# Kernel optimization log

Measured on AMD Instinct MI355X. Metric: run time of the kernel, lower is better.

The kernel has to match this reference:

```python
import jax
jax.config.update("jax_enable_x64", True)
import jax.numpy as jnp
import numpy as np

# --- Field setup -------------------------------------------------------------
# The original uses BLS12-381 Fr (255-bit Montgomery limbs). JAX has no native
# 256-bit ints, so the reference uses an NTT-friendly 31-bit prime with the
# same algorithmic structure (two-adic radix-2 INTT, grand products, MSM-style
# commitment reduction). Products of two residues fit in int64.
P = 2013265921          # 15 * 2^27 + 1, two-adicity 27
G = 31                  # generator of F_P^*
LOG_N = 20
N = 1 << LOG_N
W = pow(G, (P - 1) // N, P)      # primitive N-th root of unity
W_INV = pow(W, P - 2, P)
N_INV = pow(N, P - 2, P)
K1, K2, K3 = 7, 13, 17           # PLONK coset shifts for wire identities


def _bitrev_perm(n):
    logn = n.bit_length() - 1
    idx = np.arange(n, dtype=np.int64)
    rev = np.zeros(n, dtype=np.int64)
    for i in range(logn):
        rev = (rev << 1) | ((idx >> i) & 1)
    return rev


def _twiddles(n, root):
    logn = n.bit_length() - 1
    out = []
    for s in range(1, logn + 1):
        m = 1 << s
        wm = pow(root, n // m, P)
        half = m >> 1
        ws = np.empty(half, dtype=np.int64)
        w = 1
        for k in range(half):
            ws[k] = w
            w = (w * wm) % P
        out.append(jnp.asarray(ws))
    return out

_BREV = jnp.asarray(_bitrev_perm(N))
_TW_INV = _twiddles(N, W_INV)


def _ntt_core(a, tw):
    # iterative radix-2 Cooley-Tukey, fully vectorized per stage
    n = a.shape[0]
    a = a[_BREV]
    for s, ws in enumerate(tw):
        half = 1 << s
        a = a.reshape(-1, 2 * half)         # [n/(2*half), 2*half]
        u = a[:, :half]
        t = (a[:, half:] * ws[None, :]) % P
        a = jnp.concatenate([(u + t) % P, (u - t) % P], axis=1)
    return a.reshape(n)


def intt(evals):
    # inverse NTT: evaluations on the domain -> coefficients (nn.Intt)
    return (_ntt_core(evals, _TW_INV) * N_INV) % P


def inv_mod(x):
    # batch modular inverse: x^(P-2), exponent is a compile-time constant
    e = P - 2
    res = jnp.ones_like(x)
    base = x % P
    while e:
        if e & 1:
            res = (res * base) % P
        base = (base * base) % P
        e >>= 1
    return res


def cumprod_mod(x):
    return jax.lax.associative_scan(lambda a, b: (a * b) % P, x)


def shifted_cumprod(r):
    # z[0] = 1, z[i] = prod_{j<i} r[j]
    c = cumprod_mod(r)
    return jnp.concatenate([jnp.ones((1,), r.dtype), c[:-1]])


def commit(poly, ck):
    # stand-in for the KZG MSM: <poly, ck> mod P (same reduction structure)
    return jnp.sum((poly * ck) % P) % P


def perm_z(wires, sigmas, beta, gamma, omega_pows):
    # PLONK copy-constraint grand product (mod.compute_permutation_poly)
    ids = (omega_pows, (K1 * omega_pows) % P,
           (K2 * omega_pows) % P, (K3 * omega_pows) % P)
    num = jnp.ones((N,), jnp.int64)
    den = jnp.ones((N,), jnp.int64)
    for w, i, s in zip(wires, ids, sigmas):
        num = (num * ((w + (beta * i) % P + gamma) % P)) % P
        den = (den * ((w + (beta * s) % P + gamma) % P)) % P
    return shifted_cumprod((num * inv_mod(den)) % P)


def lookup_z2(f, t, h1, h2, delta, epsilon):
    # plookup grand product (mod.compute_lookup_permutation_poly)
    one_plus_d = (1 + delta) % P
    ep1d = (epsilon * one_plus_d) % P
    t_next = jnp.roll(t, -1)
    h1_next = jnp.roll(h1, -1)
    h2_next = jnp.roll(h2, -1)
    num = (one_plus_d * ((epsilon + f) % P)) % P
    num = (num * ((ep1d + t + (delta * t_next) % P) % P)) % P
    a = (ep1d + h1 + (delta * h1_next) % P) % P
    b = (ep1d + h2 + (delta * h2_next) % P) % P
    den = (a * b) % P
    return shifted_cumprod((num * inv_mod(den)) % P)


def setup_inputs() -> dict:
    key = jax.random.key(0)
    ks = jax.random.split(key, 16)
    def ri(k):
        return jax.random.randint(k, (N,), 0, P, dtype=jnp.int64)
    return {
        "w_l": ri(ks[0]), "w_r": ri(ks[1]), "w_o": ri(ks[2]), "w_4": ri(ks[3]),
        "q_lookup": jax.random.randint(ks[4], (N,), 0, 2, dtype=jnp.int64),
        "t1": ri(ks[5]), "t2": ri(ks[6]), "t3": ri(ks[7]), "t4": ri(ks[8]),
        "sigma_l": ri(ks[9]), "sigma_r": ri(ks[10]),
        "sigma_o": ri(ks[11]), "sigma_4": ri(ks[12]),
        "ck": ri(ks[13]),
        "zeta": 123457, "beta": 98765, "gamma": 54321,
        "delta": 13579, "epsilon": 24680,
    }


def reference(w_l, w_r, w_o, w_4, q_lookup, t1, t2, t3, t4,
              sigma_l, sigma_r, sigma_o, sigma_4, ck,
              zeta, beta, gamma, delta, epsilon):
    z2c = (zeta * zeta) % P
    z3c = (z2c * zeta) % P
    # zkp.compress: zeta-combine lookup table columns
    t = (t1 + (zeta * t2) % P + (z2c * t3) % P + (z3c * t4) % P) % P
    table_poly = intt(t)
    # zkp.compute_query_table: compressed wire query where selector is on,
    # padded with table values where it is off
    q = (w_l + (zeta * w_r) % P + (z2c * w_o) % P + (z3c * w_4) % P) % P
    f = jnp.where(q_lookup == 1, q, t)
    f_poly = intt(f)
    # witness INTTs
    w_l_poly = intt(w_l)
    w_r_poly = intt(w_r)
    w_o_poly = intt(w_o)
    w_4_poly = intt(w_4)
    # combine_split: sorted multiset of f union t, split alternating
    s = jnp.sort(jnp.concatenate([f, t]))
    h1, h2 = s[0::2], s[1::2]
    h1_poly = intt(h1)
    h2_poly = intt(h2)
    # domain elements 1, W, W^2, ...
    omega_pows = shifted_cumprod(jnp.full((N,), W, dtype=jnp.int64))
    z = perm_z((w_l, w_r, w_o, w_4), (sigma_l, sigma_r, sigma_o, sigma_4),
               beta, gamma, omega_pows)
    z_poly = intt(z)
    z2 = lookup_z2(f, t, h1, h2, delta, epsilon)
    z2_poly = intt(z2)
    polys = (w_l_poly, w_r_poly, w_o_poly, w_4_poly, f_poly, table_poly,
             h1_poly, h2_poly, z_poly, z2_poly)
    commits = jnp.stack([commit(p, ck) for p in polys])
    return polys + (commits,)
```

## Files before the change

kernel.cpp:

```cpp
#include <hip/hip_runtime.h>
#include <stdint.h>

#define PRIME 2013265921u
#define LOGN  20
#define NN    (1u << LOGN)

static constexpr uint64_t cpowmod(uint64_t b, uint64_t e){
  uint64_t r = 1; b %= PRIME;
  while (e){ if (e & 1) r = r * b % PRIME; b = b * b % PRIME; e >>= 1; }
  return r;
}
static constexpr uint32_t WFWD = (uint32_t)cpowmod(31u, (PRIME - 1u) >> LOGN);
static constexpr uint32_t WINV = (uint32_t)cpowmod(WFWD, PRIME - 2u);
static constexpr uint32_t NINV = (uint32_t)cpowmod(NN, PRIME - 2u);
static constexpr uint64_t MBAR = 0xFFFFFFFFFFFFFFFFull / PRIME;

__device__ uint32_t g_U[1024];
__device__ uint32_t g_V[1024];
__device__ uint2    g_TWp[1024];
__device__ uint2    g_U2p[1024];
__device__ uint32_t g_bcnt[2048];
__device__ uint32_t g_boff[2048];
__device__ uint32_t g_bcur[2048];
__device__ uint32_t g_btot[2048];
__device__ uint32_t g_bpre[2048];
__device__ unsigned long long g_commit[10];

__device__ __forceinline__ uint32_t mulmod(uint32_t a, uint32_t b){
  uint64_t t = (uint64_t)a * b;
  uint32_t q = (uint32_t)__umul64hi(t, MBAR);
  uint32_t r = (uint32_t)t - q * PRIME;
  if (r >= PRIME) r -= PRIME;
  return r;
}
__device__ __forceinline__ uint32_t shoup_mul(uint32_t a, uint32_t w, uint32_t ws){
  uint32_t q = __umulhi(a, ws);
  uint32_t r = a * w - q * PRIME;
  if (r >= PRIME) r -= PRIME;
  return r;
}
__device__ __forceinline__ uint32_t addmod(uint32_t a, uint32_t b){
  uint32_t s = a + b; return (s >= PRIME) ? s - PRIME : s;
}
__device__ __forceinline__ uint32_t submod(uint32_t a, uint32_t b){
  return (a >= b) ? (a - b) : (a + (PRIME - b));
}
__device__ __forceinline__ uint32_t addmod3(uint32_t a, uint32_t b, uint32_t c){
  return addmod(addmod(a, b), c);
}
__device__ __forceinline__ uint32_t powmod_dev(uint32_t b, uint32_t e){
  uint32_t r = 1u;
  while (e){ if (e & 1u) r = mulmod(r, b); b = mulmod(b, b); e >>= 1u; }
  return r;
}

__global__ __launch_bounds__(1024) void k_zero(){
  const uint32_t t = blockIdx.x * 1024u + threadIdx.x;
  if (t < 2048u) g_bcnt[t] = 0u;
  if (t < 10u)   g_commit[t] = 0ull;
}

__global__ __launch_bounds__(1024) void k_tables(){
  const uint32_t i = threadIdx.x;
  if (blockIdx.x == 0){
    g_U[i] = powmod_dev(WINV, i);
  } else if (blockIdx.x == 1){
    g_V[i] = powmod_dev(WINV, i << 10);
  } else if (blockIdx.x == 2){
    const uint32_t w = mulmod(NINV, powmod_dev(WINV, i));
    g_U2p[i] = make_uint2(w, (uint32_t)((((uint64_t)w) << 32) / PRIME));
  } else {
    uint32_t j;
    if      (i < 512u)  j = i;
    else if (i < 768u)  j = (i - 512u)  << 1;
    else if (i < 896u)  j = (i - 768u)  << 2;
    else if (i < 960u)  j = (i - 896u)  << 3;
    else if (i < 992u)  j = (i - 960u)  << 4;
    else if (i < 1008u) j = (i - 992u)  << 5;
    else if (i < 1016u) j = (i - 1008u) << 6;
    else if (i < 1020u) j = (i - 1016u) << 7;
    else if (i < 1022u) j = (i - 1020u) << 8;
    else                j = 0u;
    const uint32_t w = powmod_dev(WINV, j << 10);
    g_TWp[i] = make_uint2(w, (uint32_t)((((uint64_t)w) << 32) / PRIME));
  }
}

__global__ __launch_bounds__(1024) void k_elemA(
    const uint32_t* __restrict__ wl, const uint32_t* __restrict__ wr,
    const uint32_t* __restrict__ wo, const uint32_t* __restrict__ w4,
    const uint32_t* __restrict__ ql, const uint32_t* __restrict__ x1,
    const uint32_t* __restrict__ x2, const uint32_t* __restrict__ x3,
    const uint32_t* __restrict__ x4, const uint32_t* __restrict__ zeta_p,
    uint32_t* __restrict__ o32)
{
  __shared__ uint32_t hcnt[2048];
  const int t = threadIdx.x;
  hcnt[t] = 0u; hcnt[t + 1024] = 0u;
  __syncthreads();

  const uint32_t zeta = zeta_p[0];
  const uint32_t zc2 = mulmod(zeta, zeta), zc3 = mulmod(zc2, zeta);
  const uint32_t i0 = (uint32_t)blockIdx.x * 4096u + (uint32_t)t * 4u;

  uint4 vt1 = *(const uint4*)(x1 + i0);
  uint4 vt2 = *(const uint4*)(x2 + i0);
  uint4 vt3 = *(const uint4*)(x3 + i0);
  uint4 vt4 = *(const uint4*)(x4 + i0);
  uint4 vwl = *(const uint4*)(wl + i0);
  uint4 vwr = *(const uint4*)(wr + i0);
  uint4 vwo = *(const uint4*)(wo + i0);
  uint4 vw4 = *(const uint4*)(w4 + i0);
  uint4 vql = *(const uint4*)(ql + i0);

  uint32_t T1[4] = {vt1.x, vt1.y, vt1.z, vt1.w};
  uint32_t T2[4] = {vt2.x, vt2.y, vt2.z, vt2.w};
  uint32_t T3[4] = {vt3.x, vt3.y, vt3.z, vt3.w};
  uint32_t T4[4] = {vt4.x, vt4.y, vt4.z, vt4.w};
  uint32_t L1[4] = {vwl.x, vwl.y, vwl.z, vwl.w};
  uint32_t L2[4] = {vwr.x, vwr.y, vwr.z, vwr.w};
  uint32_t L3[4] = {vwo.x, vwo.y, vwo.z, vwo.w};
  uint32_t L4[4] = {vw4.x, vw4.y, vw4.z, vw4.w};
  uint32_t QL[4] = {vql.x, vql.y, vql.z, vql.w};

  uint32_t tv[4], fv[4];
  #pragma unroll
  for (int k = 0; k < 4; ++k){
    uint32_t tt = addmod(addmod(T1[k], mulmod(zeta, T2[k])),
                         addmod(mulmod(zc2, T3[k]), mulmod(zc3, T4[k])));
    uint32_t qq = addmod(addmod(L1[k], mulmod(zeta, L2[k])),
                         addmod(mulmod(zc2, L3[k]), mulmod(zc3, L4[k])));
    tv[k] = tt; fv[k] = (QL[k] == 1u) ? qq : tt;
  }
  uint4 o;
  o.x = tv[0]; o.y = tv[1]; o.z = tv[2]; o.w = tv[3];
  *(uint4*)(o32 + 5u*NN + i0) = o;
  o.x = fv[0]; o.y = fv[1]; o.z = fv[2]; o.w = fv[3];
  *(uint4*)(o32 + 4u*NN + i0) = o;

  #pragma unroll
  for (int k = 0; k < 4; ++k){ atomicAdd(&hcnt[fv[k] >> 20], 1u);
                               atomicAdd(&hcnt[tv[k] >> 20], 1u); }
  __syncthreads();
  uint32_t c0 = hcnt[t];          if (c0) atomicAdd(&g_bcnt[t], c0);
  uint32_t c1 = hcnt[t + 1024];   if (c1) atomicAdd(&g_bcnt[t + 1024], c1);
}

__global__ __launch_bounds__(1024) void k_bscan(){
  __shared__ uint32_t SA[2048], SB[2048];
  const int t = threadIdx.x;
  SA[t] = g_bcnt[t];
  SA[t + 1024] = g_bcnt[t + 1024];
  __syncthreads();
  uint32_t* sp = SA; uint32_t* dp = SB;
  for (int off = 1; off < 2048; off <<= 1){
    for (int i = t; i < 2048; i += 1024)
      dp[i] = (i >= off) ? (sp[i - off] + sp[i]) : sp[i];
    uint32_t* tmp = sp; sp = dp; dp = tmp;
    __syncthreads();
  }
  uint32_t e0 = t ? sp[t - 1] : 0u;
  uint32_t e1 = sp[t + 1023];
  g_boff[t] = e0;         g_bcur[t] = e0;
  g_boff[t + 1024] = e1;  g_bcur[t + 1024] = e1;
}

__global__ __launch_bounds__(1024) void k_scat2(uint32_t* __restrict__ o32){
  __shared__ uint32_t sorted[8192];
  __shared__ uint32_t hist[2048];
  __shared__ uint32_t SA[2048];
  __shared__ uint32_t wsum[16];
  __shared__ uint32_t gbase[2048];
  const int t = threadIdx.x;
  const uint32_t base = blockIdx.x * 8192u;

  hist[t] = 0u; hist[t + 1024] = 0u;
  __syncthreads();

  uint32_t v[8], rk[8];
  #pragma unroll
  for (int k = 0; k < 8; ++k)
    v[k] = o32[4u*NN + base + (uint32_t)t + (uint32_t)k * 1024u];
  #pragma unroll
  for (int k = 0; k < 8; ++k)
    rk[k] = atomicAdd(&hist[v[k] >> 20], 1u);
  __syncthreads();

  const uint32_t lane = (uint32_t)t & 63u, wid = (uint32_t)t >> 6;
  const uint32_t e0 = hist[2*t], e1 = hist[2*t + 1];
  const uint32_t s = e0 + e1;
  uint32_t scan = s;
  #pragma unroll
  for (int off = 1; off < 64; off <<= 1){
    uint32_t u = __shfl_up(scan, off, 64);
    if (lane >= (uint32_t)off) scan += u;
  }
  if (lane == 63u) wsum[wid] = scan;
  __syncthreads();
  if (t < 64){
    uint32_t u = (t < 16) ? wsum[t] : 0u;
    #pragma unroll
    for (int off = 1; off < 16; off <<= 1){
      uint32_t x2 = __shfl_up(u, off, 64);
      if ((uint32_t)t >= (uint32_t)off) u += x2;
    }
    if (t < 16) wsum[t] = u;
  }
  __syncthreads();
  const uint32_t wbase = wid ? wsum[wid - 1] : 0u;
  const uint32_t incl = wbase + scan;
  SA[2*t]     = incl - e1;
  SA[2*t + 1] = incl;
  __syncthreads();
  uint32_t* sp = SA;

  for (int b = t; b < 2048; b += 1024){
    uint32_t c = hist[b];
    if (c) gbase[b] = atomicAdd(&g_bcur[b], c);
  }
  __syncthreads();

  #pragma unroll
  for (int k = 0; k < 8; ++k){
    uint32_t b = v[k] >> 20;
    uint32_t ls = b ? sp[b - 1] : 0u;
    sorted[ls + rk[k]] = v[k];
  }
  __syncthreads();

  for (int i = t; i < 8192; i += 1024){
    uint32_t vv = sorted[i];
    uint32_t b = vv >> 20;
    uint32_t ls = b ? sp[b - 1] : 0u;
    o32[6u*NN + gbase[b] + (uint32_t)i - ls] = vv;
  }
}

__global__ __launch_bounds__(256) void k_bsort(uint32_t* __restrict__ o32){
  __shared__ uint32_t sorted[2048];
  __shared__ uint32_t SA[1024], SB[1024];
  __shared__ uint32_t wsum[4];
  const int b = blockIdx.x, t = threadIdx.x;
  uint32_t n = g_bcnt[b]; if (n > 2048u) n = 2048u;
  const uint32_t off = g_boff[b];

  for (int i = t; i < 1024; i += 256) SA[i] = 0u;
  __syncthreads();

  uint32_t v[8], rk[8];
  #pragma unroll
  for (int k = 0; k < 8; ++k){
    const uint32_t i = (uint32_t)t + (uint32_t)k * 256u;
    if (i < n){
      v[k] = o32[6u*NN + off + i];
      rk[k] = atomicAdd(&SA[(v[k] >> 10) & 1023u], 1u);
    }
  }
  __syncthreads();

  const uint32_t lane = (uint32_t)t & 63u, wid = (uint32_t)t >> 6;
  const uint32_t h0 = SA[4*t], h1 = SA[4*t + 1], h2 = SA[4*t + 2], h3 = SA[4*t + 3];
  const uint32_t s = h0 + h1 + h2 + h3;
  uint32_t scan = s;
  #pragma unroll
  for (int o = 1; o < 64; o <<= 1){
    uint32_t u = __shfl_up(scan, o, 64);
    if (lane >= (uint32_t)o) scan += u;
  }
  if (lane == 63u) wsum[wid] = scan;
  __syncthreads();
  if (t < 64){
    uint32_t u = (t < 4) ? wsum[t] : 0u;
    #pragma unroll
    for (int o = 1; o < 4; o <<= 1){
      uint32_t x2 = __shfl_up(u, o, 64);
      if ((uint32_t)t >= (uint32_t)o) u += x2;
    }
    if (t < 4) wsum[t] = u;
  }
  __syncthreads();
  const uint32_t wbase = wid ? wsum[wid - 1] : 0u;
  const uint32_t incl = wbase + scan;
  SB[4*t + 3] = incl;
  SB[4*t + 2] = incl - h3;
  SB[4*t + 1] = incl - h3 - h2;
  SB[4*t + 0] = incl - h3 - h2 - h1;
  __syncthreads();
  uint32_t* sp = SB;

  #pragma unroll
  for (int k = 0; k < 8; ++k){
    const uint32_t i = (uint32_t)t + (uint32_t)k * 256u;
    if (i < n){
      const uint32_t d = (v[k] >> 10) & 1023u;
      const uint32_t s2 = d ? sp[d - 1] : 0u;
      sorted[s2 + rk[k]] = v[k];
    }
  }
  __syncthreads();

  for (int d = t; d < 1024; d += 256){
    const uint32_t s2 = d ? sp[d - 1] : 0u;
    const uint32_t e = sp[d];
    for (uint32_t i = s2 + 1; i < e; ++i){
      const uint32_t key = sorted[i];
      uint32_t j = i;
      while (j > s2 && sorted[j - 1] > key){ sorted[j] = sorted[j - 1]; --j; }
      sorted[j] = key;
    }
  }
  __syncthreads();

  for (uint32_t i = (uint32_t)t; i < n; i += 256u) o32[6u*NN + off + i] = sorted[i];
}

__global__ __launch_bounds__(256) void k_ratio(
    const uint32_t* __restrict__ wl, const uint32_t* __restrict__ wr,
    const uint32_t* __restrict__ wo, const uint32_t* __restrict__ w4,
    const uint32_t* __restrict__ sl, const uint32_t* __restrict__ sr,
    const uint32_t* __restrict__ so, const uint32_t* __restrict__ s4,
    const uint32_t* __restrict__ beta_p, const uint32_t* __restrict__ gamma_p,
    const uint32_t* __restrict__ delta_p, const uint32_t* __restrict__ eps_p,
    uint32_t* __restrict__ o32)
{
  __shared__ uint32_t SA[256], SB[256];
  const int blk = blockIdx.x, t = threadIdx.x;
  const int second = blk >> 10;
  const uint32_t base = ((uint32_t)(blk & 1023) << 10) + ((uint32_t)t << 2);
  uint32_t num[4], den[4];
  if (!second){
    const uint32_t beta = beta_p[0], gamma = gamma_p[0];
    #pragma unroll
    for (int k = 0; k < 4; ++k){
      uint32_t i = base + (uint32_t)k;
      uint32_t e = (NN - i) & (NN - 1u);
      uint32_t om = mulmod(g_U[e & 1023u], g_V[e >> 10]);
      uint32_t bo = mulmod(beta, om);
      uint32_t n = addmod3(wl[i], bo, gamma);
      n = mulmod(n, addmod3(wr[i], mulmod(7u,  bo), gamma));
      n = mulmod(n, addmod3(wo[i], mulmod(13u, bo), gamma));
      n = mulmod(n, addmod3(w4[i], mulmod(17u, bo), gamma));
      uint32_t d = addmod3(wl[i], mulmod(beta, sl[i]), gamma);
      d = mulmod(d, addmod3(wr[i], mulmod(beta, sr[i]), gamma));
      d = mulmod(d, addmod3(wo[i], mulmod(beta, so[i]), gamma));
      d = mulmod(d, addmod3(w4[i], mulmod(beta, s4[i]), gamma));
      num[k] = n; den[k] = d;
    }
  } else {
    const uint32_t del = delta_p[0], ep = eps_p[0];
    const uint32_t opd = addmod(1u, del), ep1d = mulmod(ep, opd);
    #pragma unroll
    for (int k = 0; k < 4; ++k){
      uint32_t i = base + (uint32_t)k;
      uint32_t fi = o32[4u*NN + i], ti = o32[5u*NN + i];
      uint32_t tn = o32[5u*NN + ((i + 1u) & (NN - 1u))];
      uint32_t h1  = o32[6u*NN + 2u*i];
      uint32_t h2  = o32[6u*NN + 2u*i + 1u];
      uint32_t h1n = o32[6u*NN + ((2u*i + 2u) & (2u*NN - 1u))];
      uint32_t h2n = o32[6u*NN + ((2u*i + 3u) & (2u*NN - 1u))];
      uint32_t n = mulmod(opd, addmod(ep, fi));
      n = mulmod(n, addmod3(ep1d, ti, mulmod(del, tn)));
      uint32_t d = mulmod(addmod3(ep1d, h1, mulmod(del, h1n)),
                          addmod3(ep1d, h2, mulmod(del, h2n)));
      num[k] = n; den[k] = d;
    }
  }
  uint32_t r[4];
  if (den[0] && den[1] && den[2] && den[3]){
    uint32_t p0 = den[0];
    uint32_t p1 = mulmod(p0, den[1]);
    uint32_t p2 = mulmod(p1, den[2]);
    uint32_t p3 = mulmod(p2, den[3]);
    uint32_t iv = powmod_dev(p3, PRIME - 2u);
    uint32_t i3 = mulmod(iv, p2); iv = mulmod(iv, den[3]);
    uint32_t i2 = mulmod(iv, p1); iv = mulmod(iv, den[2]);
    uint32_t i1 = mulmod(iv, p0); iv = mulmod(iv, den[1]);
    r[0] = mulmod(num[0], iv);
    r[1] = mulmod(num[1], i1);
    r[2] = mulmod(num[2], i2);
    r[3] = mulmod(num[3], i3);
  } else {
    #pragma unroll
    for (int k = 0; k < 4; ++k) r[k] = mulmod(num[k], powmod_dev(den[k], PRIME - 2u));
  }
  uint32_t tp = mulmod(mulmod(r[0], r[1]), mulmod(r[2], r[3]));
  SA[t] = tp; __syncthreads();
  uint32_t* sp = SA; uint32_t* dp = SB;
  for (int off = 1; off < 256; off <<= 1){
    dp[t] = (t >= off) ? mulmod(sp[t - off], sp[t]) : sp[t];
    uint32_t* tmp = sp; sp = dp; dp = tmp;
    __syncthreads();
  }
  if (t == 255) g_btot[blk] = sp[255];
  uint32_t run = t ? sp[t - 1] : 1u;
  const uint32_t zo = 8u*NN + ((uint32_t)blk << 10) + ((uint32_t)t << 2);
  o32[zo + 0] = run; run = mulmod(run, r[0]);
  o32[zo + 1] = run; run = mulmod(run, r[1]);
  o32[zo + 2] = run; run = mulmod(run, r[2]);
  o32[zo + 3] = run;
}

__global__ __launch_bounds__(1024) void k_btscan(){
  __shared__ uint32_t SA[1024], SB[1024];
  const int a = blockIdx.x, t = threadIdx.x;
  SA[t] = g_btot[a * 1024 + t];
  __syncthreads();
  uint32_t* sp = SA; uint32_t* dp = SB;
  for (int off = 1; off < 1024; off <<= 1){
    dp[t] = (t >= off) ? mulmod(sp[t - off], sp[t]) : sp[t];
    uint32_t* tmp = sp; sp = dp; dp = tmp;
    __syncthreads();
  }
  g_bpre[a * 1024 + t] = t ? sp[t - 1] : 1u;
}

__global__ __launch_bounds__(256) void k_apply(uint32_t* __restrict__ o32){
  const uint32_t g = blockIdx.x * 256u + threadIdx.x;
  const uint32_t base = g << 2;
  const uint32_t m = g_bpre[base >> 10];
  uint4* zz = (uint4*)(o32 + 8u*NN);
  uint4 v = zz[g];
  v.x = mulmod(v.x, m); v.y = mulmod(v.y, m); v.z = mulmod(v.z, m); v.w = mulmod(v.w, m);
  zz[g] = v;
}

struct Desc  { const uint32_t* p; uint32_t stride; uint32_t off; };
struct Descs { Desc d[10]; };
struct Map   { int g[10]; };

#define SWZ(i, c) (((i) << 4) + ((c) ^ (((i) >> 1) & 15)))

__device__ __forceinline__ void ntt1024_reg(uint32_t x[16], int l,
                                            const uint2* __restrict__ sTW){
  #pragma unroll
  for (int st = 9; st >= 6; --st){
    const int bb = 1 << (st - 6);
    const int base = (st == 9) ? 0 : (st == 8) ? 512 : (st == 7) ? 768 : 896;
    #pragma unroll
    for (int r = 0; r < 16; ++r){
      if ((r & bb) == 0){
        const int r2 = r | bb;
        const uint32_t u = x[r], v = x[r2];
        const uint2 wv = sTW[base + ((r & (bb - 1)) << 6) + l];
        x[r]  = addmod(u, v);
        x[r2] = shoup_mul(submod(u, v), wv.x, wv.y);
      }
    }
  }
  #pragma unroll
  for (int st = 5; st >= 0; --st){
    const int h = 1 << st;
    const int base = (st == 5) ? 960 : (st == 4) ? 992 : (st == 3) ? 1008
                   : (st == 2) ? 1016 : (st == 1) ? 1020 : 1022;
    const uint2 wv = sTW[base + (l & (h - 1))];
    const bool hi = (l & h) != 0;
    #pragma unroll
    for (int r = 0; r < 16; ++r){
      const uint32_t y = __shfl_xor(x[r], h, 64);
      const uint32_t a = addmod(x[r], y);
      const uint32_t b = shoup_mul(submod(y, x[r]), wv.x, wv.y);
      x[r] = hi ? b : a;
    }
  }
}

__global__ __launch_bounds__(1024, 8) void k_intt1(Descs ds, uint32_t* __restrict__ mid){
  __shared__ uint32_t tile[16384];
  __shared__ uint2 sTW[1024];
  const int arr = blockIdx.x >> 6;
  const int c0 = (blockIdx.x & 63) << 4;
  const Desc de = ds.d[arr];
  const int t = threadIdx.x;
  sTW[t] = g_TWp[t];
  if (de.stride == 1u){
    #pragma unroll
    for (int it = 0; it < 4; ++it){
      const int row = (it << 8) + (t >> 2);
      const int cb = (t & 3) << 2;
      uint4 v = *(const uint4*)(de.p + (size_t)row * 1024u + (uint32_t)(c0 + cb));
      tile[SWZ(row, cb + 0)] = v.x; tile[SWZ(row, cb + 1)] = v.y;
      tile[SWZ(row, cb + 2)] = v.z; tile[SWZ(row, cb + 3)] = v.w;
    }
  } else {
    #pragma unroll
    for (int it = 0; it < 4; ++it){
      const int row = (it << 8) + (t >> 2);
      const int cb = (t & 3) << 2;
      const size_t b0 = 2u * ((size_t)row * 1024u + (uint32_t)(c0 + cb));
      uint4 a0 = *(const uint4*)(de.p + b0);
      uint4 a1 = *(const uint4*)(de.p + b0 + 4u);
      if (de.off == 0u){
        tile[SWZ(row, cb + 0)] = a0.x; tile[SWZ(row, cb + 1)] = a0.z;
        tile[SWZ(row, cb + 2)] = a1.x; tile[SWZ(row, cb + 3)] = a1.z;
      } else {
        tile[SWZ(row, cb + 0)] = a0.y; tile[SWZ(row, cb + 1)] = a0.w;
        tile[SWZ(row, cb + 2)] = a1.y; tile[SWZ(row, cb + 3)] = a1.w;
      }
    }
  }
  __syncthreads();
  const int w = t >> 6, l = t & 63;
  uint32_t x[16];
  #pragma unroll
  for (int r = 0; r < 16; ++r) x[r] = tile[SWZ(l + (r << 6), w)];
  ntt1024_reg(x, l, sTW);
  const uint32_t i1g = (uint32_t)(c0 + w);
  const uint32_t rl = __brev((uint32_t)l) >> 26;
  #pragma unroll
  for (int r = 0; r < 16; ++r){
    const uint32_t rr = __brev((uint32_t)r) >> 28;
    const uint32_t j1 = (rl << 4) | rr;
    const uint32_t e = j1 * i1g;
    const uint2 wa = g_U2p[e & 1023u];
    const uint32_t hv = e >> 10;
    const uint2 wb = sTW[hv & 511u];
    uint32_t wbw = wb.x, wbs = wb.y;
    if (hv & 512u){ wbw = PRIME - wbw; wbs = ~wbs; }
    x[r] = shoup_mul(x[r], wa.x, wa.y);
    x[r] = shoup_mul(x[r], wbw, wbs);
  }
  __syncthreads();
  #pragma unroll
  for (int r = 0; r < 16; ++r) tile[SWZ(l + (r << 6), w)] = x[r];
  __syncthreads();
  uint32_t* mo = mid + ((size_t)arr << 20);
  #pragma unroll
  for (int it = 0; it < 4; ++it){
    const int row = (it << 8) + (t >> 2);
    const int cb = (t & 3) << 2;
    uint4 v;
    v.x = tile[SWZ(row, cb + 0)]; v.y = tile[SWZ(row, cb + 1)];
    v.z = tile[SWZ(row, cb + 2)]; v.w = tile[SWZ(row, cb + 3)];
    *(uint4*)(mo + (size_t)row * 1024u + (uint32_t)(c0 + cb)) = v;
  }
}

__global__ __launch_bounds__(1024, 8) void k_intt2(const uint32_t* __restrict__ mid,
                                                   uint32_t* __restrict__ o32,
                                                   const uint32_t* __restrict__ ck,
                                                   Map mp){
  __shared__ uint32_t tile[16384];
  __shared__ uint2 sTW[1024];
  const int arrL = blockIdx.x >> 6;
  const int m0 = (blockIdx.x & 63) << 4;
  const int t = threadIdx.x;
  const int w = t >> 6, l = t & 63;
  const int gidx = mp.g[arrL];
  const uint32_t* mi = mid + ((size_t)arrL << 20);
  const uint32_t p = __brev((uint32_t)(m0 + w)) >> 22;
  sTW[t] = g_TWp[t];
  #pragma unroll
  for (int it = 0; it < 4; ++it){
    const int kb = (it << 8) + (l << 2);
    uint4 v = *(const uint4*)(mi + p * 1024u + (uint32_t)kb);
    tile[SWZ(kb + 0, w)] = v.x; tile[SWZ(kb + 1, w)] = v.y;
    tile[SWZ(kb + 2, w)] = v.z; tile[SWZ(kb + 3, w)] = v.w;
  }
  __syncthreads();
  uint32_t x[16];
  #pragma unroll
  for (int r = 0; r < 16; ++r) x[r] = tile[SWZ(l + (r << 6), w)];
  ntt1024_reg(x, l, sTW);
  __syncthreads();
  #pragma unroll
  for (int r = 0; r < 16; ++r) tile[SWZ(l + (r << 6), w)] = x[r];
  __syncthreads();
  unsigned long long acc = 0ull;
  uint32_t* oa = o32 + ((size_t)gidx << 20);
  #pragma unroll
  for (int it = 0; it < 4; ++it){
    const int j2 = (it << 8) + (t >> 2);
    const int rb = (t & 3) << 2;
    const uint32_t q = __brev((uint32_t)j2) >> 22;
    uint4 v;
    v.x = tile[SWZ((int)q, rb + 0)]; v.y = tile[SWZ((int)q, rb + 1)];
    v.z = tile[SWZ((int)q, rb + 2)]; v.w = tile[SWZ((int)q, rb + 3)];
    const uint32_t oi = (uint32_t)j2 * 1024u + (uint32_t)(m0 + rb);
    *(uint4*)(oa + oi) = v;
    uint4 cv = *(const uint4*)(ck + oi);
    acc += (unsigned long long)mulmod(v.x, cv.x);
    acc += (unsigned long long)mulmod(v.y, cv.y);
    acc += (unsigned long long)mulmod(v.z, cv.z);
    acc += (unsigned long long)mulmod(v.w, cv.w);
  }
  #pragma unroll
  for (int off = 32; off >= 1; off >>= 1) acc += __shfl_down(acc, off, 64);
  __syncthreads();
  unsigned long long* redw = (unsigned long long*)tile;
  if (l == 0) redw[w] = acc;
  __syncthreads();
  if (t < 64){
    unsigned long long s = (t < 16) ? redw[t] : 0ull;
    #pragma unroll
    for (int off = 8; off >= 1; off >>= 1) s += __shfl_down(s, off, 64);
    if (t == 0) atomicAdd(&g_commit[gidx], s);
  }
}

__global__ __launch_bounds__(256) void k_brev(const uint32_t* __restrict__ src,
                                              uint32_t stride, uint32_t off,
                                              uint32_t* __restrict__ dst){
  const uint32_t i = blockIdx.x * 256u + threadIdx.x;
  const uint32_t r = __brev(i) >> 12;
  dst[i] = src[(size_t)r * stride + off];
}

__global__ __launch_bounds__(1024) void k_stage09(uint32_t* __restrict__ wk){
  __shared__ uint32_t sm[1024];
  const int t = threadIdx.x;
  const uint32_t gbase = blockIdx.x * 1024u;
  sm[t] = wk[gbase + t];
  __syncthreads();
  for (int s = 0; s <= 9; ++s){
    if (t < 512){
      const int half = 1 << s;
      const int k = t & (half - 1);
      const int i0 = ((t >> s) << (s + 1)) | k;
      const int i1 = i0 + half;
      const uint32_t tw = g_V[(uint32_t)k << (9 - s)];
      const uint32_t u = sm[i0];
      const uint32_t tv = mulmod(sm[i1], tw);
      sm[i0] = addmod(u, tv);
      sm[i1] = submod(u, tv);
    }
    __syncthreads();
  }
  wk[gbase + t] = sm[t];
}

__global__ __launch_bounds__(256) void k_stage(uint32_t* __restrict__ wk, int s){
  const uint32_t q = blockIdx.x * 256u + threadIdx.x;
  const uint32_t half = 1u << s;
  const uint32_t k = q & (half - 1u);
  const uint32_t i0 = ((q >> s) << (s + 1)) | k;
  const uint32_t i1 = i0 + half;
  const uint32_t e = k << (19 - s);
  const uint32_t tw = mulmod(g_U[e & 1023u], g_V[e >> 10]);
  const uint32_t u = wk[i0];
  const uint32_t tv = mulmod(wk[i1], tw);
  wk[i0] = addmod(u, tv);
  wk[i1] = submod(u, tv);
}

__global__ __launch_bounds__(1024) void k_scale_commit(const uint32_t* __restrict__ src,
                                                       uint32_t* dst,
                                                       const uint32_t* __restrict__ ck,
                                                       int cidx){
  __shared__ unsigned long long red[1024];
  const uint32_t i = blockIdx.x * 1024u + threadIdx.x;
  const uint32_t val = mulmod(src[i], NINV);
  dst[i] = val;
  red[threadIdx.x] = (unsigned long long)mulmod(val, ck[i]);
  __syncthreads();
  for (int s = 512; s > 0; s >>= 1){
    if ((int)threadIdx.x < s) red[threadIdx.x] += red[threadIdx.x + s];
    __syncthreads();
  }
  if (threadIdx.x == 0) atomicAdd(&g_commit[cidx], red[0]);
}

__global__ void k_final(uint32_t* __restrict__ out){
  const int i = threadIdx.x;
  if (i < 10) out[(size_t)10 * NN + i] = (uint32_t)(g_commit[i] % (unsigned long long)PRIME);
}

extern "C" void kernel_launch(void* const* d_in, const int* in_sizes, int n_in,
                              void* d_out, int out_size, void* d_ws, size_t ws_size,
                              hipStream_t stream)
{
  const uint32_t* wl   = (const uint32_t*)d_in[0];
  const uint32_t* wr   = (const uint32_t*)d_in[1];
  const uint32_t* wo   = (const uint32_t*)d_in[2];
  const uint32_t* w4   = (const uint32_t*)d_in[3];
  const uint32_t* ql   = (const uint32_t*)d_in[4];
  const uint32_t* t1   = (const uint32_t*)d_in[5];
  const uint32_t* t2   = (const uint32_t*)d_in[6];
  const uint32_t* t3   = (const uint32_t*)d_in[7];
  const uint32_t* t4   = (const uint32_t*)d_in[8];
  const uint32_t* sl   = (const uint32_t*)d_in[9];
  const uint32_t* sr   = (const uint32_t*)d_in[10];
  const uint32_t* so   = (const uint32_t*)d_in[11];
  const uint32_t* s4   = (const uint32_t*)d_in[12];
  const uint32_t* ck   = (const uint32_t*)d_in[13];
  const uint32_t* zeta = (const uint32_t*)d_in[14];
  const uint32_t* beta = (const uint32_t*)d_in[15];
  const uint32_t* gam  = (const uint32_t*)d_in[16];
  const uint32_t* del  = (const uint32_t*)d_in[17];
  const uint32_t* eps  = (const uint32_t*)d_in[18];
  uint32_t* o32 = (uint32_t*)d_out;
  (void)in_sizes; (void)n_in; (void)out_size;

  k_zero  <<<2, 1024, 0, stream>>>();
  k_tables<<<4, 1024, 0, stream>>>();
  k_elemA <<<256, 1024, 0, stream>>>(wl, wr, wo, w4, ql, t1, t2, t3, t4, zeta, o32);
  k_bscan <<<1, 1024, 0, stream>>>();
  k_scat2 <<<256, 1024, 0, stream>>>(o32);
  k_bsort <<<1920, 256, 0, stream>>>(o32);
  k_ratio <<<2048, 256, 0, stream>>>(wl, wr, wo, w4, sl, sr, so, s4, beta, gam, del, eps, o32);
  k_btscan<<<2, 1024, 0, stream>>>();
  k_apply <<<2048, 256, 0, stream>>>(o32);

  Desc ds[10];
  ds[0] = { wl,          1u, 0u };
  ds[1] = { wr,          1u, 0u };
  ds[2] = { wo,          1u, 0u };
  ds[3] = { w4,          1u, 0u };
  ds[4] = { o32 + 4u*NN, 1u, 0u };
  ds[5] = { o32 + 5u*NN, 1u, 0u };
  ds[6] = { o32 + 6u*NN, 2u, 0u };
  ds[7] = { o32 + 6u*NN, 2u, 1u };
  ds[8] = { o32 + 8u*NN, 1u, 0u };
  ds[9] = { o32 + 9u*NN, 1u, 0u };

  const size_t wsWords = ws_size / 4u;
  if (wsWords >= 2ull * NN){
    static const int ord[10] = {6,7, 4,5, 8,9, 0,1, 2,3};
    const int chunk = (wsWords >= 10ull * NN) ? 10 : 2;
    uint32_t* mid = (uint32_t*)d_ws;
    for (int s0 = 0; s0 < 10; s0 += chunk){
      const int cnt = (10 - s0 < chunk) ? (10 - s0) : chunk;
      Descs sub; Map mp;
      for (int a = 0; a < 10; ++a){
        const int g = ord[(a < cnt) ? s0 + a : s0];
        sub.d[a] = ds[g]; mp.g[a] = g;
      }
      k_intt1<<<64 * cnt, 1024, 0, stream>>>(sub, mid);
      k_intt2<<<64 * cnt, 1024, 0, stream>>>(mid, o32, ck, mp);
    }
  } else {
    auto run_intt = [&](const Desc& d, uint32_t workSlot, int dstSlot){
      uint32_t* wk = o32 + (size_t)workSlot * NN;
      k_brev   <<<4096, 256, 0, stream>>>(d.p, d.stride, d.off, wk);
      k_stage09<<<1024, 1024, 0, stream>>>(wk);
      for (int s = 10; s < 20; ++s)
        k_stage<<<2048, 256, 0, stream>>>(wk, s);
      k_scale_commit<<<1024, 1024, 0, stream>>>(wk, o32 + (size_t)dstSlot * NN, ck, dstSlot);
    };
    k_brev<<<4096, 256, 0, stream>>>(ds[6].p, 2u, 0u, o32 + 0u*NN);
    k_brev<<<4096, 256, 0, stream>>>(ds[7].p, 2u, 1u, o32 + 1u*NN);
    {
      uint32_t* wk0 = o32;
      uint32_t* wk1 = o32 + NN;
      k_stage09<<<1024, 1024, 0, stream>>>(wk0);
      for (int s = 10; s < 20; ++s) k_stage<<<2048, 256, 0, stream>>>(wk0, s);
      k_scale_commit<<<1024, 1024, 0, stream>>>(wk0, o32 + 6u*NN, ck, 6);
      k_stage09<<<1024, 1024, 0, stream>>>(wk1);
      for (int s = 10; s < 20; ++s) k_stage<<<2048, 256, 0, stream>>>(wk1, s);
      k_scale_commit<<<1024, 1024, 0, stream>>>(wk1, o32 + 7u*NN, ck, 7);
    }
    run_intt(ds[4], 0u, 4);
    run_intt(ds[5], 1u, 5);
    run_intt(ds[8], 0u, 8);
    run_intt(ds[9], 1u, 9);
    run_intt(ds[0], 0u, 0);
    run_intt(ds[1], 1u, 1);
    run_intt(ds[2], 2u, 2);
    run_intt(ds[3], 3u, 3);
  }
  k_final<<<1, 64, 0, stream>>>(o32);
}
```

Baseline: 201.1 us.

## Halve INTT block size with 8-column tiles and batch 8 elements per thread in ratio kernel

The four-step INTT kernels now use 512-thread blocks that loop over two 8-column tiles, with a smaller 8192-word shared tile and a new 8-wide swizzle. This shrinks per-block LDS and register pressure so more blocks can stay resident, and keeps twiddles loaded once per block. The ratio/grand-product kernel handles 8 elements per thread with one batched inversion for all 8, halving the number of modular exponentiations and the number of block totals the follow-up scan must combine. The cost is more sequential work and register use per thread in the ratio kernel, plus an extra barrier per tile loop in the INTT kernels.

```diff
diff --git a/kernel.cpp b/kernel.cpp
--- a/kernel.cpp
+++ b/kernel.cpp
@@ -325,13 +325,13 @@
 {
   __shared__ uint32_t SA[256], SB[256];
   const int blk = blockIdx.x, t = threadIdx.x;
-  const int second = blk >> 10;
-  const uint32_t base = ((uint32_t)(blk & 1023) << 10) + ((uint32_t)t << 2);
-  uint32_t num[4], den[4];
+  const int second = blk >> 9;
+  const uint32_t base = ((uint32_t)(blk & 511) << 11) + ((uint32_t)t << 3);
+  uint32_t num[8], den[8];
   if (!second){
     const uint32_t beta = beta_p[0], gamma = gamma_p[0];
     #pragma unroll
-    for (int k = 0; k < 4; ++k){
+    for (int k = 0; k < 8; ++k){
       uint32_t i = base + (uint32_t)k;
       uint32_t e = (NN - i) & (NN - 1u);
       uint32_t om = mulmod(g_U[e & 1023u], g_V[e >> 10]);
@@ -350,7 +350,7 @@
     const uint32_t del = delta_p[0], ep = eps_p[0];
     const uint32_t opd = addmod(1u, del), ep1d = mulmod(ep, opd);
     #pragma unroll
-    for (int k = 0; k < 4; ++k){
+    for (int k = 0; k < 8; ++k){
       uint32_t i = base + (uint32_t)k;
       uint32_t fi = o32[4u*NN + i], ti = o32[5u*NN + i];
       uint32_t tn = o32[5u*NN + ((i + 1u) & (NN - 1u))];
@@ -365,25 +365,29 @@
       num[k] = n; den[k] = d;
     }
   }
-  uint32_t r[4];
-  if (den[0] && den[1] && den[2] && den[3]){
-    uint32_t p0 = den[0];
-    uint32_t p1 = mulmod(p0, den[1]);
-    uint32_t p2 = mulmod(p1, den[2]);
-    uint32_t p3 = mulmod(p2, den[3]);
-    uint32_t iv = powmod_dev(p3, PRIME - 2u);
-    uint32_t i3 = mulmod(iv, p2); iv = mulmod(iv, den[3]);
-    uint32_t i2 = mulmod(iv, p1); iv = mulmod(iv, den[2]);
-    uint32_t i1 = mulmod(iv, p0); iv = mulmod(iv, den[1]);
+  bool ok = true;
+  #pragma unroll
+  for (int k = 0; k < 8; ++k) ok = ok && (den[k] != 0u);
+  uint32_t r[8];
+  if (ok){
+    uint32_t pp[8];
+    pp[0] = den[0];
+    #pragma unroll
+    for (int k = 1; k < 8; ++k) pp[k] = mulmod(pp[k-1], den[k]);
+    uint32_t iv = powmod_dev(pp[7], PRIME - 2u);
+    #pragma unroll
+    for (int k = 7; k >= 1; --k){
+      r[k] = mulmod(num[k], mulmod(iv, pp[k-1]));
+      iv = mulmod(iv, den[k]);
+    }
     r[0] = mulmod(num[0], iv);
-    r[1] = mulmod(num[1], i1);
-    r[2] = mulmod(num[2], i2);
-    r[3] = mulmod(num[3], i3);
   } else {
     #pragma unroll
-    for (int k = 0; k < 4; ++k) r[k] = mulmod(num[k], powmod_dev(den[k], PRIME - 2u));
-  }
-  uint32_t tp = mulmod(mulmod(r[0], r[1]), mulmod(r[2], r[3]));
+    for (int k = 0; k < 8; ++k) r[k] = mulmod(num[k], powmod_dev(den[k], PRIME - 2u));
+  }
+  uint32_t tp = r[0];
+  #pragma unroll
+  for (int k = 1; k < 8; ++k) tp = mulmod(tp, r[k]);
   SA[t] = tp; __syncthreads();
   uint32_t* sp = SA; uint32_t* dp = SB;
   for (int off = 1; off < 256; off <<= 1){
@@ -393,31 +397,32 @@
   }
   if (t == 255) g_btot[blk] = sp[255];
   uint32_t run = t ? sp[t - 1] : 1u;
-  const uint32_t zo = 8u*NN + ((uint32_t)blk << 10) + ((uint32_t)t << 2);
-  o32[zo + 0] = run; run = mulmod(run, r[0]);
-  o32[zo + 1] = run; run = mulmod(run, r[1]);
-  o32[zo + 2] = run; run = mulmod(run, r[2]);
-  o32[zo + 3] = run;
-}
-
-__global__ __launch_bounds__(1024) void k_btscan(){
-  __shared__ uint32_t SA[1024], SB[1024];
+  const uint32_t zo = 8u*NN + ((uint32_t)second << 20) + base;
+  #pragma unroll
+  for (int k = 0; k < 8; ++k){
+    o32[zo + (uint32_t)k] = run;
+    run = mulmod(run, r[k]);
+  }
+}
+
+__global__ __launch_bounds__(512) void k_btscan(){
+  __shared__ uint32_t SA[512], SB[512];
   const int a = blockIdx.x, t = threadIdx.x;
-  SA[t] = g_btot[a * 1024 + t];
+  SA[t] = g_btot[a * 512 + t];
   __syncthreads();
   uint32_t* sp = SA; uint32_t* dp = SB;
-  for (int off = 1; off < 1024; off <<= 1){
+  for (int off = 1; off < 512; off <<= 1){
     dp[t] = (t >= off) ? mulmod(sp[t - off], sp[t]) : sp[t];
     uint32_t* tmp = sp; sp = dp; dp = tmp;
     __syncthreads();
   }
-  g_bpre[a * 1024 + t] = t ? sp[t - 1] : 1u;
+  g_bpre[a * 512 + t] = t ? sp[t - 1] : 1u;
 }
 
 __global__ __launch_bounds__(256) void k_apply(uint32_t* __restrict__ o32){
   const uint32_t g = blockIdx.x * 256u + threadIdx.x;
   const uint32_t base = g << 2;
-  const uint32_t m = g_bpre[base >> 10];
+  const uint32_t m = g_bpre[base >> 11];
   uint4* zz = (uint4*)(o32 + 8u*NN);
   uint4 v = zz[g];
   v.x = mulmod(v.x, m); v.y = mulmod(v.y, m); v.z = mulmod(v.z, m); v.w = mulmod(v.w, m);
@@ -428,7 +433,7 @@
 struct Descs { Desc d[10]; };
 struct Map   { int g[10]; };
 
-#define SWZ(i, c) (((i) << 4) + ((c) ^ (((i) >> 1) & 15)))
+#define SWZ8(i, c) (((i) << 3) + ((c) ^ (((i) >> 2) & 7)))
 
 __device__ __forceinline__ void ntt1024_reg(uint32_t x[16], int l,
                                             const uint2* __restrict__ sTW){
@@ -464,135 +469,142 @@
   }
 }
 
-__global__ __launch_bounds__(1024, 8) void k_intt1(Descs ds, uint32_t* __restrict__ mid){
-  __shared__ uint32_t tile[16384];
+__global__ __launch_bounds__(512, 8) void k_intt1(Descs ds, uint32_t* __restrict__ mid){
+  __shared__ uint32_t tile[8192];
   __shared__ uint2 sTW[1024];
-  const int arr = blockIdx.x >> 6;
-  const int c0 = (blockIdx.x & 63) << 4;
-  const Desc de = ds.d[arr];
   const int t = threadIdx.x;
   sTW[t] = g_TWp[t];
-  if (de.stride == 1u){
+  sTW[t + 512] = g_TWp[t + 512];
+  const int arr = blockIdx.x >> 6;
+  const Desc de = ds.d[arr];
+  const int w = t >> 6, l = t & 63;
+  uint32_t* mo = mid + ((size_t)arr << 20);
+
+  for (int ti = 0; ti < 2; ++ti){
+    const int c0 = ((((blockIdx.x & 63) << 1) | ti) << 3);
+    if (ti) __syncthreads();
+    if (de.stride == 1u){
+      #pragma unroll
+      for (int it = 0; it < 4; ++it){
+        const int row = (it << 8) + (t >> 1);
+        const int cb = (t & 1) << 2;
+        uint4 v = *(const uint4*)(de.p + (size_t)row * 1024u + (uint32_t)(c0 + cb));
+        tile[SWZ8(row, cb + 0)] = v.x; tile[SWZ8(row, cb + 1)] = v.y;
+        tile[SWZ8(row, cb + 2)] = v.z; tile[SWZ8(row, cb + 3)] = v.w;
+      }
+    } else {
+      #pragma unroll
+      for (int it = 0; it < 4; ++it){
+        const int row = (it << 8) + (t >> 1);
+        const int cb = (t & 1) << 2;
+        const size_t b0 = 2u * ((size_t)row * 1024u + (uint32_t)(c0 + cb));
+        uint4 a0 = *(const uint4*)(de.p + b0);
+        uint4 a1 = *(const uint4*)(de.p + b0 + 4u);
+        if (de.off == 0u){
+          tile[SWZ8(row, cb + 0)] = a0.x; tile[SWZ8(row, cb + 1)] = a0.z;
+          tile[SWZ8(row, cb + 2)] = a1.x; tile[SWZ8(row, cb + 3)] = a1.z;
+        } else {
+          tile[SWZ8(row, cb + 0)] = a0.y; tile[SWZ8(row, cb + 1)] = a0.w;
+          tile[SWZ8(row, cb + 2)] = a1.y; tile[SWZ8(row, cb + 3)] = a1.w;
+        }
+      }
+    }
+    __syncthreads();
+    uint32_t x[16];
+    #pragma unroll
+    for (int r = 0; r < 16; ++r) x[r] = tile[SWZ8(l + (r << 6), w)];
+    ntt1024_reg(x, l, sTW);
+    const uint32_t i1g = (uint32_t)(c0 + w);
+    const uint32_t rl = __brev((uint32_t)l) >> 26;
+    #pragma unroll
+    for (int r = 0; r < 16; ++r){
+      const uint32_t rr = __brev((uint32_t)r) >> 28;
+      const uint32_t j1 = (rl << 4) | rr;
+      const uint32_t e = j1 * i1g;
+      const uint2 wa = g_U2p[e & 1023u];
+      const uint32_t hv = e >> 10;
+      const uint2 wb = sTW[hv & 511u];
+      uint32_t wbw = wb.x, wbs = wb.y;
+      if (hv & 512u){ wbw = PRIME - wbw; wbs = ~wbs; }
+      x[r] = shoup_mul(x[r], wa.x, wa.y);
+      x[r] = shoup_mul(x[r], wbw, wbs);
+    }
+    #pragma unroll
+    for (int r = 0; r < 16; ++r) tile[SWZ8(l + (r << 6), w)] = x[r];
+    __syncthreads();
     #pragma unroll
     for (int it = 0; it < 4; ++it){
-      const int row = (it << 8) + (t >> 2);
-      const int cb = (t & 3) << 2;
-      uint4 v = *(const uint4*)(de.p + (size_t)row * 1024u + (uint32_t)(c0 + cb));
-      tile[SWZ(row, cb + 0)] = v.x; tile[SWZ(row, cb + 1)] = v.y;
-      tile[SWZ(row, cb + 2)] = v.z; tile[SWZ(row, cb + 3)] = v.w;
-    }
-  } else {
+      const int row = (it << 8) + (t >> 1);
+      const int cb = (t & 1) << 2;
+      uint4 v;
+      v.x = tile[SWZ8(row, cb + 0)]; v.y = tile[SWZ8(row, cb + 1)];
+      v.z = tile[SWZ8(row, cb + 2)]; v.w = tile[SWZ8(row, cb + 3)];
+      *(uint4*)(mo + (size_t)row * 1024u + (uint32_t)(c0 + cb)) = v;
+    }
+  }
+}
+
+__global__ __launch_bounds__(512, 8) void k_intt2(const uint32_t* __restrict__ mid,
+                                                  uint32_t* __restrict__ o32,
+                                                  const uint32_t* __restrict__ ck,
+                                                  Map mp){
+  __shared__ uint32_t tile[8192];
+  __shared__ uint2 sTW[1024];
+  __shared__ unsigned long long redw[8];
+  const int t = threadIdx.x;
+  sTW[t] = g_TWp[t];
+  sTW[t + 512] = g_TWp[t + 512];
+  const int arrL = blockIdx.x >> 6;
+  const int gidx = mp.g[arrL];
+  const int w = t >> 6, l = t & 63;
+  const uint32_t* mi = mid + ((size_t)arrL << 20);
+  uint32_t* oa = o32 + ((size_t)gidx << 20);
+  unsigned long long acc = 0ull;
+
+  for (int ti = 0; ti < 2; ++ti){
+    const int m0 = ((((blockIdx.x & 63) << 1) | ti) << 3);
+    if (ti) __syncthreads();
+    const uint32_t p = __brev((uint32_t)(m0 + w)) >> 22;
     #pragma unroll
     for (int it = 0; it < 4; ++it){
-      const int row = (it << 8) + (t >> 2);
-      const int cb = (t & 3) << 2;
-      const size_t b0 = 2u * ((size_t)row * 1024u + (uint32_t)(c0 + cb));
-      uint4 a0 = *(const uint4*)(de.p + b0);
-      uint4 a1 = *(const uint4*)(de.p + b0 + 4u);
-      if (de.off == 0u){
-        tile[SWZ(row, cb + 0)] = a0.x; tile[SWZ(row, cb + 1)] = a0.z;
-        tile[SWZ(row, cb + 2)] = a1.x; tile[SWZ(row, cb + 3)] = a1.z;
-      } else {
-        tile[SWZ(row, cb + 0)] = a0.y; tile[SWZ(row, cb + 1)] = a0.w;
-        tile[SWZ(row, cb + 2)] = a1.y; tile[SWZ(row, cb + 3)] = a1.w;
-      }
-    }
-  }
-  __syncthreads();
-  const int w = t >> 6, l = t & 63;
-  uint32_t x[16];
-  #pragma unroll
-  for (int r = 0; r < 16; ++r) x[r] = tile[SWZ(l + (r << 6), w)];
-  ntt1024_reg(x, l, sTW);
-  const uint32_t i1g = (uint32_t)(c0 + w);
-  const uint32_t rl = __brev((uint32_t)l) >> 26;
-  #pragma unroll
-  for (int r = 0; r < 16; ++r){
-    const uint32_t rr = __brev((uint32_t)r) >> 28;
-    const uint32_t j1 = (rl << 4) | rr;
-    const uint32_t e = j1 * i1g;
-    const uint2 wa = g_U2p[e & 1023u];
-    const uint32_t hv = e >> 10;
-    const uint2 wb = sTW[hv & 511u];
-    uint32_t wbw = wb.x, wbs = wb.y;
-    if (hv & 512u){ wbw = PRIME - wbw; wbs = ~wbs; }
-    x[r] = shoup_mul(x[r], wa.x, wa.y);
-    x[r] = shoup_mul(x[r], wbw, wbs);
-  }
-  __syncthreads();
-  #pragma unroll
-  for (int r = 0; r < 16; ++r) tile[SWZ(l + (r << 6), w)] = x[r];
-  __syncthreads();
-  uint32_t* mo = mid + ((size_t)arr << 20);
-  #pragma unroll
-  for (int it = 0; it < 4; ++it){
-    const int row = (it << 8) + (t >> 2);
-    const int cb = (t & 3) << 2;
-    uint4 v;
-    v.x = tile[SWZ(row, cb + 0)]; v.y = tile[SWZ(row, cb + 1)];
-    v.z = tile[SWZ(row, cb + 2)]; v.w = tile[SWZ(row, cb + 3)];
-    *(uint4*)(mo + (size_t)row * 1024u + (uint32_t)(c0 + cb)) = v;
-  }
-}
-
-__global__ __launch_bounds__(1024, 8) void k_intt2(const uint32_t* __restrict__ mid,
-                                                   uint32_t* __restrict__ o32,
-                                                   const uint32_t* __restrict__ ck,
-                                                   Map mp){
-  __shared__ uint32_t tile[16384];
-  __shared__ uint2 sTW[1024];
-  const int arrL = blockIdx.x >> 6;
-  const int m0 = (blockIdx.x & 63) << 4;
-  const int t = threadIdx.x;
-  const int w = t >> 6, l = t & 63;
-  const int gidx = mp.g[arrL];
-  const uint32_t* mi = mid + ((size_t)arrL << 20);
-  const uint32_t p = __brev((uint32_t)(m0 + w)) >> 22;
-  sTW[t] = g_TWp[t];
-  #pragma unroll
-  for (int it = 0; it < 4; ++it){
-    const int kb = (it << 8) + (l << 2);
-    uint4 v = *(const uint4*)(mi + p * 1024u + (uint32_t)kb);
-    tile[SWZ(kb + 0, w)] = v.x; tile[SWZ(kb + 1, w)] = v.y;
-    tile[SWZ(kb + 2, w)] = v.z; tile[SWZ(kb + 3, w)] = v.w;
-  }
-  __syncthreads();
-  uint32_t x[16];
-  #pragma unroll
-  for (int r = 0; r < 16; ++r) x[r] = tile[SWZ(l + (r << 6), w)];
-  ntt1024_reg(x, l, sTW);
-  __syncthreads();
-  #pragma unroll
-  for (int r = 0; r < 16; ++r) tile[SWZ(l + (r << 6), w)] = x[r];
-  __syncthreads();
-  unsigned long long acc = 0ull;
-  uint32_t* oa = o32 + ((size_t)gidx << 20);
-  #pragma unroll
-  for (int it = 0; it < 4; ++it){
-    const int j2 = (it << 8) + (t >> 2);
-    const int rb = (t & 3) << 2;
-    const uint32_t q = __brev((uint32_t)j2) >> 22;
-    uint4 v;
-    v.x = tile[SWZ((int)q, rb + 0)]; v.y = tile[SWZ((int)q, rb + 1)];
-    v.z = tile[SWZ((int)q, rb + 2)]; v.w = tile[SWZ((int)q, rb + 3)];
-    const uint32_t oi = (uint32_t)j2 * 1024u + (uint32_t)(m0 + rb);
-    *(uint4*)(oa + oi) = v;
-    uint4 cv = *(const uint4*)(ck + oi);
-    acc += (unsigned long long)mulmod(v.x, cv.x);
-    acc += (unsigned long long)mulmod(v.y, cv.y);
-    acc += (unsigned long long)mulmod(v.z, cv.z);
-    acc += (unsigned long long)mulmod(v.w, cv.w);
+      const int kb = (it << 8) + (l << 2);
+      uint4 v = *(const uint4*)(mi + p * 1024u + (uint32_t)kb);
+      tile[SWZ8(kb + 0, w)] = v.x; tile[SWZ8(kb + 1, w)] = v.y;
+      tile[SWZ8(kb + 2, w)] = v.z; tile[SWZ8(kb + 3, w)] = v.w;
+    }
+    __syncthreads();
+    uint32_t x[16];
+    #pragma unroll
+    for (int r = 0; r < 16; ++r) x[r] = tile[SWZ8(l + (r << 6), w)];
+    ntt1024_reg(x, l, sTW);
+    #pragma unroll
+    for (int r = 0; r < 16; ++r) tile[SWZ8(l + (r << 6), w)] = x[r];
+    __syncthreads();
+    #pragma unroll
+    for (int it = 0; it < 4; ++it){
+      const int j2 = (it << 8) + (t >> 1);
+      const int rb = (t & 1) << 2;
+      const uint32_t q = __brev((uint32_t)j2) >> 22;
+      uint4 v;
+      v.x = tile[SWZ8((int)q, rb + 0)]; v.y = tile[SWZ8((int)q, rb + 1)];
+      v.z = tile[SWZ8((int)q, rb + 2)]; v.w = tile[SWZ8((int)q, rb + 3)];
+      const uint32_t oi = (uint32_t)j2 * 1024u + (uint32_t)(m0 + rb);
+      *(uint4*)(oa + oi) = v;
+      uint4 cv = *(const uint4*)(ck + oi);
+      acc += (unsigned long long)mulmod(v.x, cv.x);
+      acc += (unsigned long long)mulmod(v.y, cv.y);
+      acc += (unsigned long long)mulmod(v.z, cv.z);
+      acc += (unsigned long long)mulmod(v.w, cv.w);
+    }
   }
   #pragma unroll
   for (int off = 32; off >= 1; off >>= 1) acc += __shfl_down(acc, off, 64);
-  __syncthreads();
-  unsigned long long* redw = (unsigned long long*)tile;
   if (l == 0) redw[w] = acc;
   __syncthreads();
   if (t < 64){
-    unsigned long long s = (t < 16) ? redw[t] : 0ull;
-    #pragma unroll
-    for (int off = 8; off >= 1; off >>= 1) s += __shfl_down(s, off, 64);
+    unsigned long long s = (t < 8) ? redw[t] : 0ull;
+    #pragma unroll
+    for (int off = 4; off >= 1; off >>= 1) s += __shfl_down(s, off, 64);
     if (t == 0) atomicAdd(&g_commit[gidx], s);
   }
 }
@@ -696,8 +708,8 @@
   k_bscan <<<1, 1024, 0, stream>>>();
   k_scat2 <<<256, 1024, 0, stream>>>(o32);
   k_bsort <<<1920, 256, 0, stream>>>(o32);
-  k_ratio <<<2048, 256, 0, stream>>>(wl, wr, wo, w4, sl, sr, so, s4, beta, gam, del, eps, o32);
-  k_btscan<<<2, 1024, 0, stream>>>();
+  k_ratio <<<1024, 256, 0, stream>>>(wl, wr, wo, w4, sl, sr, so, s4, beta, gam, del, eps, o32);
+  k_btscan<<<2, 512, 0, stream>>>();
   k_apply <<<2048, 256, 0, stream>>>(o32);
 
   Desc ds[10];
@@ -724,8 +736,8 @@
         const int g = ord[(a < cnt) ? s0 + a : s0];
         sub.d[a] = ds[g]; mp.g[a] = g;
       }
-      k_intt1<<<64 * cnt, 1024, 0, stream>>>(sub, mid);
-      k_intt2<<<64 * cnt, 1024, 0, stream>>>(mid, o32, ck, mp);
+      k_intt1<<<64 * cnt, 512, 0, stream>>>(sub, mid);
+      k_intt2<<<64 * cnt, 512, 0, stream>>>(mid, o32, ck, mp);
     }
   } else {
     auto run_intt = [&](const Desc& d, uint32_t workSlot, int dstSlot){
```

New measurement: 232.5 us. +15.6%, slower.
